# Performance work log

Measured on AMD Instinct MI355X. Metric: run time of the kernel, lower is better.

The kernel has to match this reference:

```python
import jax, jax.numpy as jnp
import numpy as np
from jax import lax

B, T, N, C_IN = 1024, 10, 113, 4
E = N * 16
INV_STD = float(1.0 / np.sqrt(1.0 + 1e-5))  # eval-mode BatchNorm, running_mean=0, running_var=1
_DN = ('NHWC', 'HWIO', 'NHWC')  # (B,T,N,C) treated as NHWC, conv kernel (kt,1,Cin,Cout)


def _tconv(x, w, b):
    # x: (B,t,N,Cin), w: (3,1,Cin,Cout) -> (B,t-2,N,Cout); == Conv2d(Cin,Cout,(1,3)) in the torch layout
    return lax.conv_general_dilated(x, w, (1, 1), 'VALID', dimension_numbers=_DN) + b


def _gated_tcn(x, wp, bp, wq, bq, wr, br):
    # TemporalConv: relu(P * sigmoid(Q) + R)
    return jax.nn.relu(_tconv(x, wp, bp) * jax.nn.sigmoid(_tconv(x, wq, bq)) + _tconv(x, wr, br))


def _stconv(x, wp1, bp1, wq1, bq1, wr1, br1, cw, cb, wp2, bp2, wq2, bq2, wr2, br2, g, beta):
    h = _gated_tcn(x, wp1, bp1, wq1, bq1, wr1, br1)
    # ChebConv with K=1: only the identity term T_0 = x -> per-node linear (edge_index unused)
    h = jax.nn.relu(h @ cw + cb)
    h = _gated_tcn(h, wp2, bp2, wq2, bq2, wr2, br2)
    # BatchNorm2d over the node dim, eval mode (mean 0, var 1)
    return h * INV_STD * g[None, None, :, None] + beta[None, None, :, None]


def setup_inputs() -> dict:
    key = jax.random.key(0)
    ks = iter(jax.random.split(key, 48))

    def nrm(shape, s=0.1):
        return jax.random.normal(next(ks), shape, jnp.float32) * s

    d = {'x': nrm((B, T, N, C_IN), 1.0),
         'edge_index': jax.random.randint(next(ks), (2, E), 0, N)}
    # STConv block 1: in=4, hidden=32, out=64, kernel_size=3, K=1
    d['a_wp'] = nrm((3, 1, 4, 32)); d['a_bp'] = nrm((32,))
    d['a_wq'] = nrm((3, 1, 4, 32)); d['a_bq'] = nrm((32,))
    d['a_wr'] = nrm((3, 1, 4, 32)); d['a_br'] = nrm((32,))
    d['a_cw'] = nrm((32, 32));      d['a_cb'] = nrm((32,))
    d['a_wp2'] = nrm((3, 1, 32, 64)); d['a_bp2'] = nrm((64,))
    d['a_wq2'] = nrm((3, 1, 32, 64)); d['a_bq2'] = nrm((64,))
    d['a_wr2'] = nrm((3, 1, 32, 64)); d['a_br2'] = nrm((64,))
    d['a_g'] = jnp.ones((N,), jnp.float32); d['a_beta'] = jnp.zeros((N,), jnp.float32)
    # STConv block 2: in=64, hidden=32, out=16, kernel_size=3, K=1
    d['b_wp'] = nrm((3, 1, 64, 32)); d['b_bp'] = nrm((32,))
    d['b_wq'] = nrm((3, 1, 64, 32)); d['b_bq'] = nrm((32,))
    d['b_wr'] = nrm((3, 1, 64, 32)); d['b_br'] = nrm((32,))
    d['b_cw'] = nrm((32, 32));       d['b_cb'] = nrm((32,))
    d['b_wp2'] = nrm((3, 1, 32, 16)); d['b_bp2'] = nrm((16,))
    d['b_wq2'] = nrm((3, 1, 32, 16)); d['b_bq2'] = nrm((16,))
    d['b_wr2'] = nrm((3, 1, 32, 16)); d['b_br2'] = nrm((16,))
    d['b_g'] = jnp.ones((N,), jnp.float32); d['b_beta'] = jnp.zeros((N,), jnp.float32)
    # 113 per-node MLPs Linear(32,64)->ReLU->Linear(64,3), stacked as batched matmuls
    d['mlp_w1'] = nrm((N, 64, 32)); d['mlp_b1'] = nrm((N, 64))
    d['mlp_w2'] = nrm((N, 3, 64));  d['mlp_b2'] = nrm((N, 3))
    return d


def reference(x, edge_index, a_wp, a_bp, a_wq, a_bq, a_wr, a_br, a_cw, a_cb,
              a_wp2, a_bp2, a_wq2, a_bq2, a_wr2, a_br2, a_g, a_beta,
              b_wp, b_bp, b_wq, b_bq, b_wr, b_br, b_cw, b_cb,
              b_wp2, b_bp2, b_wq2, b_bq2, b_wr2, b_br2, b_g, b_beta,
              mlp_w1, mlp_b1, mlp_w2, mlp_b2):
    # dropout is identity in eval mode
    h = jax.nn.relu(_stconv(x, a_wp, a_bp, a_wq, a_bq, a_wr, a_br, a_cw, a_cb,
                            a_wp2, a_bp2, a_wq2, a_bq2, a_wr2, a_br2, a_g, a_beta))
    h = jax.nn.relu(_stconv(h, b_wp, b_bp, b_wq, b_bq, b_wr, b_br, b_cw, b_cb,
                            b_wp2, b_bp2, b_wq2, b_bq2, b_wr2, b_br2, b_g, b_beta))
    # h: (B, 2, N, 16); torch flatten(x[:,:,k,:], start_dim=1) interleaves (t, c) -> (B, N, 32)
    feat = jnp.transpose(h, (0, 2, 1, 3)).reshape(h.shape[0], N, 32)
    # all 113 tiny MLPs fused into two batched matmuls
    hid = jax.nn.relu(jnp.einsum('bnf,nhf->bnh', feat, mlp_w1) + mlp_b1)
    return jnp.einsum('bnh,noh->bno', hid, mlp_w2) + mlp_b2  # (B, 113, 3)
```

## Files before the change

### kernel.cpp

```cpp
#include <hip/hip_runtime.h>
#include <hip/hip_bf16.h>
#include <math.h>


namespace {

constexpr int NT = 512;
constexpr int NP = 32;
constexpr float INV_STD = 0.9999950000374997f;

typedef __attribute__((ext_vector_type(8))) short bf16x8;
typedef __attribute__((ext_vector_type(4))) float f32x4;

constexpr int OFF_CHEB_A = 0;
constexpr int OFF_CHEB_B = 1024;
constexpr int OFF_A2     = 2048;
constexpr int OFF_B1     = 20480;
constexpr int OFF_B2     = 38912;
constexpr int OFF_S1B    = 43520;
constexpr int OFF_W1     = 46592;
constexpr int OFF_W2     = 278016;

__device__ __forceinline__ unsigned short f2bf(float f){
  unsigned int u = __float_as_uint(f);
  u += 0x7fffu + ((u >> 16) & 1u);
  return (unsigned short)(u >> 16);
}
__device__ __forceinline__ unsigned short f2bf_fast(float f){
  return __bfloat16_as_ushort(__float2bfloat16(f));
}
__device__ __forceinline__ f32x4 bcast(float v){ f32x4 r; r[0]=v; r[1]=v; r[2]=v; r[3]=v; return r; }

struct Params {
  const float *x;
  const float *awp,*abp,*awq,*abq,*awr,*abr,*acw,*acb;
  const float *awp2,*abp2,*awq2,*abq2,*awr2,*abr2,*ag,*abeta;
  const float *bwp,*bbp,*bwq,*bbq,*bwr,*bbr,*bcw,*bcb;
  const float *bwp2,*bbp2,*bwq2,*bbq2,*bwr2,*bbr2,*bg,*bbeta;
  const float *w1,*b1,*w2,*b2;
  float *out;
};

__global__ void stgcn_prep(const Params p, unsigned short* __restrict__ W)
{
  int e = blockIdx.x*256 + threadIdx.x;
  if (e < 2048){
    const float* src = (e < 1024) ? p.acw : p.bcw;
    const int j = e & 1023, co = j >> 5, k = j & 31;
    W[e] = f2bf(src[k*32 + co]);
    return;
  }
  e -= 2048;
  if (e < 18432){
    const int mat = e / 6144, j = e % 6144, co = j / 96, k = j % 96;
    const float* src = mat==0 ? p.awp2 : (mat==1 ? p.awq2 : p.awr2);
    W[OFF_A2 + e] = f2bf(src[k*64 + co]);
    return;
  }
  e -= 18432;
  if (e < 18432){
    const int mat = e / 6144, j = e % 6144, co = j / 192, k = j % 192;
    const float* src = mat==0 ? p.bwp : (mat==1 ? p.bwq : p.bwr);
    W[OFF_B1 + e] = f2bf(src[k*32 + co]);
    return;
  }
  e -= 18432;
  if (e < 4608){
    const int mat = e / 1536, j = e % 1536, co = j / 96, k = j % 96;
    const float* src = mat==0 ? p.bwp2 : (mat==1 ? p.bwq2 : p.bwr2);
    W[OFF_B2 + e] = f2bf(src[k*16 + co]);
    return;
  }
  e -= 4608;
  if (e < 3072){
    const int mat = e / 1024, j = e % 1024, co = j >> 5, k = j & 31;
    const int tt = k >> 3, ci = k & 7;
    const float* src = mat==0 ? p.awp : (mat==1 ? p.awq : p.awr);
    W[OFF_S1B + e] = (ci < 4 && tt < 3) ? f2bf(src[(tt*4+ci)*32 + co])
                                        : (unsigned short)0;
    return;
  }
  e -= 3072;
  if (e < 231424){ W[OFF_W1 + e] = f2bf(p.w1[e]); return; }
  e -= 231424;
  if (e < 21696){ W[OFF_W2 + e] = f2bf(p.w2[e]); }
}

template<int TOUT, int CIN, int COUT, int NK, int RSTI, int PSTI, int RSTO, int PSTO,
         int KP, int EPI, int MJOBS, int MSTEP, bool RELOADB>
__device__ __forceinline__ void mfma_stage(const unsigned short* __restrict__ aB,
    const unsigned short* __restrict__ gW, unsigned short* __restrict__ oB,
    const float* __restrict__ gb0, const float* __restrict__ gb1,
    const float* __restrict__ gb2,
    const int Mtile0, const int Ntile, const int lm, const int lk,
    const float bnsc, const float bnbt)
{
  const unsigned short* wbase = gW + (Ntile*16 + lm)*KP + lk*8;
  const int colbase = Ntile*16 + lk*4;
  bf16x8 wp[NK], wq[NK], wr[NK];
  if constexpr (!RELOADB){
    #pragma unroll
    for (int ks = 0; ks < NK; ++ks){
      wp[ks] = *reinterpret_cast<const bf16x8*>(wbase + ks*32);
      if constexpr (EPI >= 1){
        wq[ks] = *reinterpret_cast<const bf16x8*>(wbase +   COUT*KP + ks*32);
        wr[ks] = *reinterpret_cast<const bf16x8*>(wbase + 2*COUT*KP + ks*32);
      }
    }
  }
  const f32x4 b0v = *reinterpret_cast<const f32x4*>(gb0 + colbase);
  f32x4 b1v, b2v;
  if constexpr (EPI >= 1){
    b1v = *reinterpret_cast<const f32x4*>(gb1 + colbase);
    b2v = *reinterpret_cast<const f32x4*>(gb2 + colbase);
  }

  #pragma unroll 1
  for (int j = 0; j < MJOBS; ++j){
    const int m  = (Mtile0 + j*MSTEP)*16 + lm;
    const int pr = m / TOUT;
    const int t  = m - pr*TOUT;
    f32x4 aP = b0v, aQ, aR;
    if constexpr (EPI >= 1){ aQ = b1v; aR = b2v; }
    #pragma unroll
    for (int ks = 0; ks < NK; ++ks){
      bf16x8 fp, fq, fr;
      if constexpr (RELOADB){
        fp = *reinterpret_cast<const bf16x8*>(wbase + ks*32);
        if constexpr (EPI >= 1){
          fq = *reinterpret_cast<const bf16x8*>(wbase +   COUT*KP + ks*32);
          fr = *reinterpret_cast<const bf16x8*>(wbase + 2*COUT*KP + ks*32);
        }
      } else {
        fp = wp[ks];
        if constexpr (EPI >= 1){ fq = wq[ks]; fr = wr[ks]; }
      }
      int elem;
      if constexpr (CIN == 32) elem = pr*PSTI + (t + ks)*RSTI + lk*8;
      else                     elem = pr*PSTI + (t + (ks>>1))*RSTI + (ks&1)*32 + lk*8;
      const bf16x8 a = *reinterpret_cast<const bf16x8*>(aB + elem);
      aP = __builtin_amdgcn_mfma_f32_16x16x32_bf16(fp, a, aP, 0, 0, 0);
      if constexpr (EPI >= 1){
        aQ = __builtin_amdgcn_mfma_f32_16x16x32_bf16(fq, a, aQ, 0, 0, 0);
        aR = __builtin_amdgcn_mfma_f32_16x16x32_bf16(fr, a, aR, 0, 0, 0);
      }
    }
    ushort4 pk;
    unsigned short pv[4];
    #pragma unroll
    for (int r = 0; r < 4; ++r){
      float v;
      if constexpr (EPI == 0) v = fmaxf(aP[r], 0.f);
      else {
        const float sig = 1.f/(1.f + __expf(-aQ[r]));
        v = fmaxf(fmaf(aP[r], sig, aR[r]), 0.f);
        if constexpr (EPI == 2) v = fmaxf(fmaf(v, bnsc, bnbt), 0.f);
      }
      pv[r] = f2bf_fast(v);
    }
    pk.x = pv[0]; pk.y = pv[1]; pk.z = pv[2]; pk.w = pv[3];
    *reinterpret_cast<ushort4*>(oB + pr*PSTO + t*RSTO + colbase) = pk;
  }
}

__device__ __forceinline__ void mfma_stage4(const unsigned short* __restrict__ aB,
    const unsigned short* __restrict__ gW, unsigned short* __restrict__ oB,
    const float* __restrict__ gb0, const float* __restrict__ gb1,
    const float* __restrict__ gb2,
    const int Mtile0, const int Ntile, const int lm, const int lk)
{
  const unsigned short* wbase = gW + (Ntile*16 + lm)*192 + lk*8;
  const int colbase = Ntile*16 + lk*4;
  f32x4 aP[2], aQ[2], aR[2];
  {
    const f32x4 b0v = *reinterpret_cast<const f32x4*>(gb0 + colbase);
    const f32x4 b1v = *reinterpret_cast<const f32x4*>(gb1 + colbase);
    const f32x4 b2v = *reinterpret_cast<const f32x4*>(gb2 + colbase);
    #pragma unroll
    for (int j=0;j<2;++j){ aP[j]=b0v; aQ[j]=b1v; aR[j]=b2v; }
  }
  #pragma unroll 1
  for (int kb = 0; kb < 2; ++kb){
    bf16x8 wp[3], wq[3], wr[3];
    #pragma unroll
    for (int s = 0; s < 3; ++s){
      const int ks = kb*3 + s;
      wp[s] = *reinterpret_cast<const bf16x8*>(wbase +         ks*32);
      wq[s] = *reinterpret_cast<const bf16x8*>(wbase +  6144 + ks*32);
      wr[s] = *reinterpret_cast<const bf16x8*>(wbase + 12288 + ks*32);
    }
    #pragma unroll
    for (int j = 0; j < 2; ++j){
      const int m  = (Mtile0 + j*4)*16 + lm;
      const int pr = m >> 2, t = m & 3;
      #pragma unroll
      for (int s = 0; s < 3; ++s){
        const int ks = kb*3 + s;
        const int elem = pr*432 + (t + (ks>>1))*72 + (ks&1)*32 + lk*8;
        const bf16x8 a = *reinterpret_cast<const bf16x8*>(aB + elem);
        aP[j] = __builtin_amdgcn_mfma_f32_16x16x32_bf16(wp[s], a, aP[j], 0,0,0);
        aQ[j] = __builtin_amdgcn_mfma_f32_16x16x32_bf16(wq[s], a, aQ[j], 0,0,0);
        aR[j] = __builtin_amdgcn_mfma_f32_16x16x32_bf16(wr[s], a, aR[j], 0,0,0);
      }
    }
  }
  #pragma unroll
  for (int j = 0; j < 2; ++j){
    const int m  = (Mtile0 + j*4)*16 + lm;
    const int pr = m >> 2, t = m & 3;
    ushort4 pk;
    unsigned short pv[4];
    #pragma unroll
    for (int r = 0; r < 4; ++r){
      const float sig = 1.f/(1.f + __expf(-aQ[j][r]));
      pv[r] = f2bf_fast(fmaxf(fmaf(aP[j][r], sig, aR[j][r]), 0.f));
    }
    pk.x = pv[0]; pk.y = pv[1]; pk.z = pv[2]; pk.w = pv[3];
    *reinterpret_cast<ushort4*>(oB + pr*160 + t*40 + colbase) = pk;
  }
}

__global__ __launch_bounds__(NT, 4) void stgcn_main(const Params p,
    const unsigned short* __restrict__ W)
{
  __shared__ __align__(16) unsigned short smem[24064];
  unsigned short* const bufA = smem;
  unsigned short* const bufB = smem + 13824;
  unsigned short* const sxb  = bufB;

  const int tid = threadIdx.x;
  const int l   = tid & 63;
  const int wid = tid >> 6;
  const int lm  = l & 15;
  const int lk  = l >> 4;
  const int n   = blockIdx.x >> 5;
  const int b0  = (blockIdx.x & 31) * NP;

  for (int i = tid; i < NP*22; i += NT){
    const int pr = i / 22, c = i - pr*22;
    const int t  = c >> 1;
    unsigned short v0=0,v1=0,v2=0,v3=0;
    if (!(c & 1) && t < 10){
      const float4 xf = *reinterpret_cast<const float4*>(
          &p.x[(size_t)(((b0+pr)*10 + t)*113 + n)*4]);
      v0 = f2bf(xf.x); v1 = f2bf(xf.y); v2 = f2bf(xf.z); v3 = f2bf(xf.w);
    }
    ushort4 pk; pk.x=v0; pk.y=v1; pk.z=v2; pk.w=v3;
    *reinterpret_cast<ushort4*>(&sxb[i*4]) = pk;
  }
  __syncthreads();

  mfma_stage<8,32,32,1, 8,88, 40,320, 32, 1, 4,4, false>(
      sxb, W+OFF_S1B, bufA, p.abp, p.abq, p.abr, wid>>1, wid&1, lm, lk, 0.f, 0.f);
  __syncthreads();

  mfma_stage<8,32,32,1, 40,320, 40,320, 32, 0, 4,4, false>(
      bufA, W+OFF_CHEB_A, bufB, p.acb, p.acb, p.acb, wid>>1, wid&1, lm, lk, 0.f, 0.f);
  __syncthreads();

  {
    const float bnsc = INV_STD * p.ag[n], bnbt = p.abeta[n];
    mfma_stage<6,32,64,3, 40,320, 72,432, 96, 2, 6,2, false>(
        bufB, W+OFF_A2, bufA, p.abp2, p.abq2, p.abr2, wid>>2, wid&3, lm, lk, bnsc, bnbt);
  }
  __syncthreads();

  mfma_stage4(bufA, W+OFF_B1, bufB, p.bbp, p.bbq, p.bbr, wid>>1, wid&1, lm, lk);
  __syncthreads();

  mfma_stage<4,32,32,1, 40,160, 40,160, 32, 0, 2,4, false>(
      bufB, W+OFF_CHEB_B, bufA, p.bcb, p.bcb, p.bcb, wid>>1, wid&1, lm, lk, 0.f, 0.f);
  __syncthreads();

  if (wid < 4){
    const float bnsc = INV_STD * p.bg[n], bnbt = p.bbeta[n];
    mfma_stage<2,32,16,3, 40,160, 16,40, 96, 2, 1,1, false>(
        bufA, W+OFF_B2, bufB, p.bbp2, p.bbq2, p.bbr2, wid, 0, lm, lk, bnsc, bnbt);
  }
  __syncthreads();

  mfma_stage<1,32,64,1, 16,40, 16,72, 32, 0, 1,1, false>(
      bufB, W+OFF_W1 + n*2048, bufA, p.b1 + n*64, p.b1, p.b1, wid&1, wid>>1, lm, lk, 0.f, 0.f);
  __syncthreads();

  if (wid < 2){
    const unsigned short* WM2 = W + OFF_W2 + n*192;
    const int Mtile = wid;
    const int m = Mtile*16 + lm;
    const int lmo = (lm < 3) ? lm : 0;
    f32x4 acc = bcast(0.f);
    if (lk == 0){ acc[0]=p.b2[n*3]; acc[1]=p.b2[n*3+1]; acc[2]=p.b2[n*3+2]; }
    #pragma unroll
    for (int ks = 0; ks < 2; ++ks){
      const bf16x8 aw = *reinterpret_cast<const bf16x8*>(WM2 + lmo*64 + ks*32 + lk*8);
      const bf16x8 bh = *reinterpret_cast<const bf16x8*>(bufA + m*72 + ks*32 + lk*8);
      acc = __builtin_amdgcn_mfma_f32_16x16x32_bf16(aw, bh, acc, 0, 0, 0);
    }
    if (lk == 0){
      float* op = p.out + (size_t)((b0 + m)*113 + n)*3;
      op[0] = acc[0]; op[1] = acc[1]; op[2] = acc[2];
    }
  }
}

}

extern "C" void kernel_launch(void* const* d_in, const int* in_sizes, int n_in,
                              void* d_out, int out_size, void* d_ws, size_t ws_size,
                              hipStream_t stream) {
  (void)in_sizes; (void)n_in; (void)ws_size; (void)out_size;
  Params p;
  p.x     = (const float*)d_in[0];
  p.awp   = (const float*)d_in[2];  p.abp   = (const float*)d_in[3];
  p.awq   = (const float*)d_in[4];  p.abq   = (const float*)d_in[5];
  p.awr   = (const float*)d_in[6];  p.abr   = (const float*)d_in[7];
  p.acw   = (const float*)d_in[8];  p.acb   = (const float*)d_in[9];
  p.awp2  = (const float*)d_in[10]; p.abp2  = (const float*)d_in[11];
  p.awq2  = (const float*)d_in[12]; p.abq2  = (const float*)d_in[13];
  p.awr2  = (const float*)d_in[14]; p.abr2  = (const float*)d_in[15];
  p.ag    = (const float*)d_in[16]; p.abeta = (const float*)d_in[17];
  p.bwp   = (const float*)d_in[18]; p.bbp   = (const float*)d_in[19];
  p.bwq   = (const float*)d_in[20]; p.bbq   = (const float*)d_in[21];
  p.bwr   = (const float*)d_in[22]; p.bbr   = (const float*)d_in[23];
  p.bcw   = (const float*)d_in[24]; p.bcb   = (const float*)d_in[25];
  p.bwp2  = (const float*)d_in[26]; p.bbp2  = (const float*)d_in[27];
  p.bwq2  = (const float*)d_in[28]; p.bbq2  = (const float*)d_in[29];
  p.bwr2  = (const float*)d_in[30]; p.bbr2  = (const float*)d_in[31];
  p.bg    = (const float*)d_in[32]; p.bbeta = (const float*)d_in[33];
  p.w1    = (const float*)d_in[34]; p.b1    = (const float*)d_in[35];
  p.w2    = (const float*)d_in[36]; p.b2    = (const float*)d_in[37];
  p.out   = (float*)d_out;

  unsigned short* W = (unsigned short*)d_ws;

  stgcn_prep<<<1171, 256, 0, stream>>>(p, W);

  const int tiles = 113 * 32;
  stgcn_main<<<tiles, NT, 0, stream>>>(p, W);
}
```

Measured before the change: 145.8 us.

## Fuse stage-1 gated conv with Cheb linear and tail stages per-wave

Stage 1's gated temporal conv and the ChebConv linear are fused per wave. Each wave computes its own row tiles and passes them through a private LDS scratch, which removes a block-wide barrier and one full buffer round trip. The final block-2 gated conv, MLP layer 1 and MLP layer 2 are likewise fused per wave over 4 batch rows each, dropping two barriers and letting all 8 waves work instead of 4 or 2. Stage A2 switches to reloading weights per job (RELOADB=true) to cut register pressure. The tail wastes MFMA lanes, since only 8 or 4 of 16 rows are valid, and weight reloads add global/L2 traffic.

```diff
diff --git a/kernel.cpp b/kernel.cpp
--- a/kernel.cpp
+++ b/kernel.cpp
@@ -114,7 +114,6 @@
     b1v = *reinterpret_cast<const f32x4*>(gb1 + colbase);
     b2v = *reinterpret_cast<const f32x4*>(gb2 + colbase);
   }
-
   #pragma unroll 1
   for (int j = 0; j < MJOBS; ++j){
     const int m  = (Mtile0 + j*MSTEP)*16 + lm;
@@ -226,7 +225,7 @@
   __shared__ __align__(16) unsigned short smem[24064];
   unsigned short* const bufA = smem;
   unsigned short* const bufB = smem + 13824;
-  unsigned short* const sxb  = bufB;
+  unsigned short* const sxbA = bufA + 11008;
 
   const int tid = threadIdx.x;
   const int l   = tid & 63;
@@ -246,21 +245,66 @@
       v0 = f2bf(xf.x); v1 = f2bf(xf.y); v2 = f2bf(xf.z); v3 = f2bf(xf.w);
     }
     ushort4 pk; pk.x=v0; pk.y=v1; pk.z=v2; pk.w=v3;
-    *reinterpret_cast<ushort4*>(&sxb[i*4]) = pk;
+    *reinterpret_cast<ushort4*>(&sxbA[i*4]) = pk;
   }
   __syncthreads();
 
-  mfma_stage<8,32,32,1, 8,88, 40,320, 32, 1, 4,4, false>(
-      sxb, W+OFF_S1B, bufA, p.abp, p.abq, p.abr, wid>>1, wid&1, lm, lk, 0.f, 0.f);
-  __syncthreads();
-
-  mfma_stage<8,32,32,1, 40,320, 40,320, 32, 0, 4,4, false>(
-      bufA, W+OFF_CHEB_A, bufB, p.acb, p.acb, p.acb, wid>>1, wid&1, lm, lk, 0.f, 0.f);
+  {
+    unsigned short* bw = bufA + wid*640;
+    bf16x8 bact[2];
+    int prs[2], tss[2];
+    #pragma unroll
+    for (int mt = 0; mt < 2; ++mt){
+      const int m = (wid*2+mt)*16 + lm;
+      prs[mt] = m >> 3; tss[mt] = m & 7;
+      bact[mt] = *reinterpret_cast<const bf16x8*>(
+          sxbA + prs[mt]*88 + tss[mt]*8 + lk*8);
+    }
+    #pragma unroll 1
+    for (int mt = 0; mt < 2; ++mt){
+      #pragma unroll
+      for (int Nt = 0; Nt < 2; ++Nt){
+        const unsigned short* wb = W + OFF_S1B + (Nt*16+lm)*32 + lk*8;
+        const bf16x8 wp = *reinterpret_cast<const bf16x8*>(wb);
+        const bf16x8 wq = *reinterpret_cast<const bf16x8*>(wb + 1024);
+        const bf16x8 wr = *reinterpret_cast<const bf16x8*>(wb + 2048);
+        const int cb = Nt*16 + lk*4;
+        f32x4 aP = *reinterpret_cast<const f32x4*>(p.abp + cb);
+        f32x4 aQ = *reinterpret_cast<const f32x4*>(p.abq + cb);
+        f32x4 aR = *reinterpret_cast<const f32x4*>(p.abr + cb);
+        aP = __builtin_amdgcn_mfma_f32_16x16x32_bf16(wp, bact[mt], aP, 0,0,0);
+        aQ = __builtin_amdgcn_mfma_f32_16x16x32_bf16(wq, bact[mt], aQ, 0,0,0);
+        aR = __builtin_amdgcn_mfma_f32_16x16x32_bf16(wr, bact[mt], aR, 0,0,0);
+        unsigned short pv[4];
+        #pragma unroll
+        for (int r = 0; r < 4; ++r){
+          const float sig = 1.f/(1.f + __expf(-aQ[r]));
+          pv[r] = f2bf_fast(fmaxf(fmaf(aP[r], sig, aR[r]), 0.f));
+        }
+        ushort4 pk; pk.x=pv[0]; pk.y=pv[1]; pk.z=pv[2]; pk.w=pv[3];
+        *reinterpret_cast<ushort4*>(bw + lm*40 + cb) = pk;
+      }
+      const bf16x8 bh = *reinterpret_cast<const bf16x8*>(bw + lm*40 + lk*8);
+      #pragma unroll
+      for (int Nt = 0; Nt < 2; ++Nt){
+        const bf16x8 wc = *reinterpret_cast<const bf16x8*>(
+            W + OFF_CHEB_A + (Nt*16+lm)*32 + lk*8);
+        const int cb = Nt*16 + lk*4;
+        f32x4 acc = *reinterpret_cast<const f32x4*>(p.acb + cb);
+        acc = __builtin_amdgcn_mfma_f32_16x16x32_bf16(wc, bh, acc, 0,0,0);
+        unsigned short pv[4];
+        #pragma unroll
+        for (int r = 0; r < 4; ++r) pv[r] = f2bf_fast(fmaxf(acc[r], 0.f));
+        ushort4 pk; pk.x=pv[0]; pk.y=pv[1]; pk.z=pv[2]; pk.w=pv[3];
+        *reinterpret_cast<ushort4*>(bufB + prs[mt]*320 + tss[mt]*40 + cb) = pk;
+      }
+    }
+  }
   __syncthreads();
 
   {
     const float bnsc = INV_STD * p.ag[n], bnbt = p.abeta[n];
-    mfma_stage<6,32,64,3, 40,320, 72,432, 96, 2, 6,2, false>(
+    mfma_stage<6,32,64,3, 40,320, 72,432, 96, 2, 6,2, true>(
         bufB, W+OFF_A2, bufA, p.abp2, p.abq2, p.abr2, wid>>2, wid&3, lm, lk, bnsc, bnbt);
   }
   __syncthreads();
@@ -272,33 +316,82 @@
       bufB, W+OFF_CHEB_B, bufA, p.bcb, p.bcb, p.bcb, wid>>1, wid&1, lm, lk, 0.f, 0.f);
   __syncthreads();
 
-  if (wid < 4){
-    const float bnsc = INV_STD * p.bg[n], bnbt = p.bbeta[n];
-    mfma_stage<2,32,16,3, 40,160, 16,40, 96, 2, 1,1, false>(
-        bufA, W+OFF_B2, bufB, p.bbp2, p.bbq2, p.bbr2, wid, 0, lm, lk, bnsc, bnbt);
-  }
-  __syncthreads();
-
-  mfma_stage<1,32,64,1, 16,40, 16,72, 32, 0, 1,1, false>(
-      bufB, W+OFF_W1 + n*2048, bufA, p.b1 + n*64, p.b1, p.b1, wid&1, wid>>1, lm, lk, 0.f, 0.f);
-  __syncthreads();
-
-  if (wid < 2){
-    const unsigned short* WM2 = W + OFF_W2 + n*192;
-    const int Mtile = wid;
-    const int m = Mtile*16 + lm;
-    const int lmo = (lm < 3) ? lm : 0;
-    f32x4 acc = bcast(0.f);
-    if (lk == 0){ acc[0]=p.b2[n*3]; acc[1]=p.b2[n*3+1]; acc[2]=p.b2[n*3+2]; }
-    #pragma unroll
-    for (int ks = 0; ks < 2; ++ks){
-      const bf16x8 aw = *reinterpret_cast<const bf16x8*>(WM2 + lmo*64 + ks*32 + lk*8);
-      const bf16x8 bh = *reinterpret_cast<const bf16x8*>(bufA + m*72 + ks*32 + lk*8);
-      acc = __builtin_amdgcn_mfma_f32_16x16x32_bf16(aw, bh, acc, 0, 0, 0);
-    }
-    if (lk == 0){
-      float* op = p.out + (size_t)((b0 + m)*113 + n)*3;
-      op[0] = acc[0]; op[1] = acc[1]; op[2] = acc[2];
+  {
+    unsigned short* h4W  = bufB + wid*416;
+    unsigned short* hidW = h4W + 128;
+    const int lmv = lm & 7;
+    const int prL = lmv >> 1, t6 = lmv & 1;
+    const int prG = wid*4 + prL;
+
+    {
+      const unsigned short* wb = W + OFF_B2 + lm*96 + lk*8;
+      bf16x8 wp[3], wq[3], wr[3];
+      #pragma unroll
+      for (int ks = 0; ks < 3; ++ks){
+        wp[ks] = *reinterpret_cast<const bf16x8*>(wb +        ks*32);
+        wq[ks] = *reinterpret_cast<const bf16x8*>(wb + 1536 + ks*32);
+        wr[ks] = *reinterpret_cast<const bf16x8*>(wb + 3072 + ks*32);
+      }
+      const int cb = lk*4;
+      f32x4 aP = *reinterpret_cast<const f32x4*>(p.bbp2 + cb);
+      f32x4 aQ = *reinterpret_cast<const f32x4*>(p.bbq2 + cb);
+      f32x4 aR = *reinterpret_cast<const f32x4*>(p.bbr2 + cb);
+      #pragma unroll
+      for (int ks = 0; ks < 3; ++ks){
+        const int elem = prG*160 + (t6 + ks)*40 + lk*8;
+        const bf16x8 a = *reinterpret_cast<const bf16x8*>(bufA + elem);
+        aP = __builtin_amdgcn_mfma_f32_16x16x32_bf16(wp[ks], a, aP, 0,0,0);
+        aQ = __builtin_amdgcn_mfma_f32_16x16x32_bf16(wq[ks], a, aQ, 0,0,0);
+        aR = __builtin_amdgcn_mfma_f32_16x16x32_bf16(wr[ks], a, aR, 0,0,0);
+      }
+      if (lm < 8){
+        const float bns = INV_STD * p.bg[n], bnb = p.bbeta[n];
+        unsigned short pv[4];
+        #pragma unroll
+        for (int r = 0; r < 4; ++r){
+          const float sig = 1.f/(1.f + __expf(-aQ[r]));
+          float v = fmaxf(fmaf(aP[r], sig, aR[r]), 0.f);
+          v = fmaxf(fmaf(v, bns, bnb), 0.f);
+          pv[r] = f2bf_fast(v);
+        }
+        ushort4 pk; pk.x=pv[0]; pk.y=pv[1]; pk.z=pv[2]; pk.w=pv[3];
+        *reinterpret_cast<ushort4*>(h4W + prL*32 + t6*16 + cb) = pk;
+      }
+    }
+    {
+      const bf16x8 bh = *reinterpret_cast<const bf16x8*>(h4W + (lm&3)*32 + lk*8);
+      #pragma unroll
+      for (int Nt = 0; Nt < 4; ++Nt){
+        const bf16x8 wf = *reinterpret_cast<const bf16x8*>(
+            W + OFF_W1 + n*2048 + (Nt*16+lm)*32 + lk*8);
+        const int cb = Nt*16 + lk*4;
+        f32x4 acc = *reinterpret_cast<const f32x4*>(p.b1 + n*64 + cb);
+        acc = __builtin_amdgcn_mfma_f32_16x16x32_bf16(wf, bh, acc, 0,0,0);
+        if (lm < 4){
+          unsigned short pv[4];
+          #pragma unroll
+          for (int r = 0; r < 4; ++r) pv[r] = f2bf_fast(fmaxf(acc[r], 0.f));
+          ushort4 pk; pk.x=pv[0]; pk.y=pv[1]; pk.z=pv[2]; pk.w=pv[3];
+          *reinterpret_cast<ushort4*>(hidW + lm*72 + cb) = pk;
+        }
+      }
+    }
+    {
+      const unsigned short* WM2 = W + OFF_W2 + n*192;
+      const int lmo = (lm < 3) ? lm : 0;
+      f32x4 acc = bcast(0.f);
+      if (lk == 0){ acc[0]=p.b2[n*3]; acc[1]=p.b2[n*3+1]; acc[2]=p.b2[n*3+2]; }
+      #pragma unroll
+      for (int ks = 0; ks < 2; ++ks){
+        const bf16x8 aw = *reinterpret_cast<const bf16x8*>(WM2 + lmo*64 + ks*32 + lk*8);
+        const bf16x8 bh = *reinterpret_cast<const bf16x8*>(hidW + (lm&3)*72 + ks*32 + lk*8);
+        acc = __builtin_amdgcn_mfma_f32_16x16x32_bf16(aw, bh, acc, 0,0,0);
+      }
+      if (lk == 0 && lm < 4){
+        const int b = b0 + wid*4 + lm;
+        float* op = p.out + ((size_t)b*113 + n)*3;
+        op[0] = acc[0]; op[1] = acc[1]; op[2] = acc[2];
+      }
     }
   }
 }
```

New measurement: 176.5 us. +21.0%, slower.
